# Performance work log

Measured on AMD Instinct MI355X. Metric: run time of the kernel, lower is better.

Reference implementation:

```python
import jax, jax.numpy as jnp
import numpy as np

H = 256        # hidden_size
MAX_LEN = 200  # position table has MAX_LEN+1 rows
B = 4096       # number of sessions


def setup_inputs() -> dict:
    rng = np.random.RandomState(0)
    # ragged session lengths in [10, 100)
    seq_len = rng.randint(10, 100, size=B).astype(np.int64)
    T = int(seq_len.sum())
    # reverse positions: len-1, ..., 1, 0 per session (as the torch code uses)
    reverse_pos = np.concatenate([np.arange(l - 1, -1, -1) for l in seq_len]).astype(np.int64)

    key = jax.random.key(0)
    ks = jax.random.split(key, 8)
    def lin(k, fin, fout):
        # torch Linear init ~ U(-1/sqrt(fin), 1/sqrt(fin)); store as [fin, fout]
        lim = 1.0 / np.sqrt(fin)
        kw, kb = jax.random.split(k)
        W = jax.random.uniform(kw, (fin, fout), jnp.float32, -lim, lim)
        b = jax.random.uniform(kb, (fout,), jnp.float32, -lim, lim)
        return W, b

    hidden = jax.random.normal(ks[0], (T, H), jnp.float32)
    pos_table = jax.random.normal(ks[1], (MAX_LEN + 1, H), jnp.float32)
    W_pos, b_pos = lin(ks[2], 2 * H, H)   # W_pos_inter
    W1, b1 = lin(ks[3], H, H)             # W_1_inter
    W2, b2 = lin(ks[4], H, H)             # W_2_inter
    qw, qb = lin(ks[5], H, 1)             # q_inter

    return {
        "hidden": hidden,
        "pos_table": pos_table,
        "W_pos": W_pos, "b_pos": b_pos,
        "W1": W1, "b1": b1,
        "W2": W2, "b2": b2,
        "qw": qw, "qb": qb,
        "seq_len": jnp.asarray(seq_len),
        "reverse_pos": jnp.asarray(reverse_pos),
    }


def reference(hidden, pos_table, W_pos, b_pos, W1, b1, W2, b2, qw, qb, seq_len, reverse_pos):
    T = hidden.shape[0]
    nb = seq_len.shape[0]
    # segment id per token (sessions are contiguous)
    seg = jnp.repeat(jnp.arange(nb), seq_len, total_repeat_length=T)  # [T]
    # per-session mean, gathered back per token (v_mean_repeat_concat)
    sess_mean = jax.ops.segment_sum(hidden, seg, num_segments=nb)
    sess_mean = sess_mean / seq_len[:, None].astype(hidden.dtype)
    v_mean = sess_mean[seg]                                           # [T, H]
    # position-augmented hidden: tanh(W_pos_inter([hidden; pos_emb]))
    pos_emb = pos_table[reverse_pos]                                  # [T, H]
    pos_hidden = jnp.tanh(jnp.concatenate([hidden, pos_emb], -1) @ W_pos + b_pos)
    # alpha = q_inter(sigmoid(W_1_inter(v_mean) + W_2_inter(pos_hidden)))
    gate = jax.nn.sigmoid(v_mean @ W1 + b1 + pos_hidden @ W2 + b2)
    alpha = gate @ qw + qb                                            # [T, 1]
    # per-session weighted sum of hidden
    h_s = jax.ops.segment_sum(alpha * hidden, seg, num_segments=nb)   # [B, H]
    return h_s
```

## Files before the change

### kernel.cpp

```cpp
#include <hip/hip_runtime.h>
#include <hip/hip_bf16.h>
#include <stdint.h>

#define HD 256
#define BM 128
#define MAXS 16
#define APAD 8
#define ASTRIDE (HD + APAD)
#define USTRIDE (HD + 4)

typedef __bf16 bf16x8 __attribute__((ext_vector_type(8)));
typedef float f32x4 __attribute__((ext_vector_type(4)));
typedef unsigned short ushort8v __attribute__((ext_vector_type(8)));
typedef unsigned short us4 __attribute__((ext_vector_type(4)));

__device__ __forceinline__ unsigned short f2bf(float f) {
    unsigned int x = __float_as_uint(f);
    unsigned int r = (x + 0x7FFFu + ((x >> 16) & 1u)) >> 16;
    return (unsigned short)r;
}
__device__ __forceinline__ float bf2f(unsigned short u) {
    return __uint_as_float(((unsigned)u) << 16);
}

__global__ void prep_kernel(const int* __restrict__ seq_len, int* __restrict__ offsets, int B,
                            int* __restrict__ grp_off, int* __restrict__ grp_meta,
                            const float* __restrict__ Wp, const float* __restrict__ W1,
                            const float* __restrict__ W2,
                            unsigned short* __restrict__ WphT, unsigned short* __restrict__ WpbT,
                            unsigned short* __restrict__ W1T, unsigned short* __restrict__ W2T) {
    int tid = threadIdx.x;
    if (blockIdx.x == 0) {
        __shared__ int sums[256];
        int per = (B + 255) / 256;
        int b0 = tid * per;
        int local[32];
        int tot = 0;
        for (int i = 0; i < per && i < 32; ++i) {
            int b = b0 + i;
            int v = (b < B) ? seq_len[b] : 0;
            local[i] = tot;
            tot += v;
        }
        sums[tid] = tot;
        __syncthreads();
        for (int off = 1; off < 256; off <<= 1) {
            int v = (tid >= off) ? sums[tid - off] : 0;
            __syncthreads();
            sums[tid] += v;
            __syncthreads();
        }
        int start = sums[tid] - tot;
        for (int i = 0; i < per && i < 32; ++i) {
            int b = b0 + i;
            if (b < B) offsets[b] = start + local[i];
        }
        if (tid == 255) offsets[B] = sums[255];

        int starts[32];
        int ng = 0;
        {
            int cur = 0, cnt = 0;
            for (int i = 0; i < per && i < 32; ++i) {
                int b = b0 + i;
                if (b >= B) break;
                int nxt = (i + 1 < per && i + 1 < 32) ? local[i + 1] : tot;
                int len = nxt - local[i];
                if (i == 0 || cur + len > BM || cnt == MAXS) { starts[ng++] = b; cur = 0; cnt = 0; }
                cur += len; cnt++;
            }
        }
        __syncthreads();
        sums[tid] = ng;
        __syncthreads();
        for (int off = 1; off < 256; off <<= 1) {
            int v = (tid >= off) ? sums[tid - off] : 0;
            __syncthreads();
            sums[tid] += v;
            __syncthreads();
        }
        int gbase = sums[tid] - ng;
        for (int j = 0; j < ng; ++j) grp_off[gbase + j] = starts[j];
        if (tid == 255) { grp_meta[0] = sums[255]; grp_off[sums[255]] = B; }
    } else {
        __shared__ unsigned short tile[64][72];
        int bid = blockIdx.x - 1;
        const float* src;
        unsigned short* dst;
        int k0, n0, kk;
        if (bid < 32) {
            int tk = bid >> 2, tn = bid & 3;
            src = Wp; k0 = tk * 64; n0 = tn * 64;
            if (k0 < 256) { dst = WphT; kk = k0; }
            else          { dst = WpbT; kk = k0 - 256; }
        } else if (bid < 48) {
            int b2 = bid - 32;
            src = W1; k0 = (b2 >> 2) * 64; n0 = (b2 & 3) * 64;
            dst = W1T; kk = k0;
        } else {
            int b2 = bid - 48;
            src = W2; k0 = (b2 >> 2) * 64; n0 = (b2 & 3) * 64;
            dst = W2T; kk = k0;
        }
        {
            int col = tid & 63;
            int rbase = tid >> 6;
            #pragma unroll
            for (int i = 0; i < 16; ++i) {
                int lrow = rbase + 4 * i;
                tile[lrow][col] = f2bf(src[(size_t)(k0 + lrow) * HD + n0 + col]);
            }
        }
        __syncthreads();
        {
            int nl = tid >> 2;
            int kc0 = (tid & 3) * 16;
            #pragma unroll
            for (int j = 0; j < 4; ++j) {
                int kc = kc0 + 4 * j;
                us4 v;
                v[0] = tile[kc + 0][nl];
                v[1] = tile[kc + 1][nl];
                v[2] = tile[kc + 2][nl];
                v[3] = tile[kc + 3][nl];
                *reinterpret_cast<us4*>(dst + (size_t)(n0 + nl) * HD + kk + kc) = v;
            }
        }
    }
}

__global__ __launch_bounds__(256) void p2_kernel(
    const float* __restrict__ pos_table, int Mp,
    const unsigned short* __restrict__ WpbT, const float* __restrict__ bp,
    float* __restrict__ P2) {
    __shared__ __align__(16) unsigned short As[16][ASTRIDE];
    int tid = threadIdx.x;
    int m0 = blockIdx.x * 16;
    {
        int row = tid >> 4;
        int colg = (tid & 15) * 16;
        int m = m0 + row;
        float4 f[4] = {{0,0,0,0},{0,0,0,0},{0,0,0,0},{0,0,0,0}};
        if (m < Mp) {
            const float4* p = reinterpret_cast<const float4*>(pos_table + (size_t)m * HD + colg);
            f[0] = p[0]; f[1] = p[1]; f[2] = p[2]; f[3] = p[3];
        }
        ushort8v v0, v1;
        v0[0]=f2bf(f[0].x); v0[1]=f2bf(f[0].y); v0[2]=f2bf(f[0].z); v0[3]=f2bf(f[0].w);
        v0[4]=f2bf(f[1].x); v0[5]=f2bf(f[1].y); v0[6]=f2bf(f[1].z); v0[7]=f2bf(f[1].w);
        v1[0]=f2bf(f[2].x); v1[1]=f2bf(f[2].y); v1[2]=f2bf(f[2].z); v1[3]=f2bf(f[2].w);
        v1[4]=f2bf(f[3].x); v1[5]=f2bf(f[3].y); v1[6]=f2bf(f[3].z); v1[7]=f2bf(f[3].w);
        *reinterpret_cast<ushort8v*>(&As[row][colg])     = v0;
        *reinterpret_cast<ushort8v*>(&As[row][colg + 8]) = v1;
    }
    __syncthreads();

    int wave = tid >> 6, lane = tid & 63, quad = lane >> 4, cc = lane & 15;
    int nb = wave * 64;
    f32x4 acc4[4];
    for (int i = 0; i < 4; ++i) acc4[i] = (f32x4){0.f, 0.f, 0.f, 0.f};
    bf16x8 wfp[4];
    for (int nf = 0; nf < 4; ++nf)
        wfp[nf] = *reinterpret_cast<const bf16x8*>(WpbT + (size_t)(nb + nf * 16 + cc) * HD + quad * 8);
    for (int kc8 = 0; kc8 < 8; ++kc8) {
        int kc = kc8 * 32;
        bf16x8 wfc[4];
        for (int nf = 0; nf < 4; ++nf) wfc[nf] = wfp[nf];
        if (kc8 < 7)
            for (int nf = 0; nf < 4; ++nf)
                wfp[nf] = *reinterpret_cast<const bf16x8*>(WpbT + (size_t)(nb + nf * 16 + cc) * HD + kc + 32 + quad * 8);
        bf16x8 af = *reinterpret_cast<const bf16x8*>(&As[cc][kc + quad * 8]);
        for (int nf = 0; nf < 4; ++nf)
            acc4[nf] = __builtin_amdgcn_mfma_f32_16x16x32_bf16(af, wfc[nf], acc4[nf], 0, 0, 0);
    }
    for (int nf = 0; nf < 4; ++nf)
        for (int r = 0; r < 4; ++r) {
            int row = m0 + quad * 4 + r;
            int col = nb + nf * 16 + cc;
            if (row < Mp) P2[(size_t)row * HD + col] = acc4[nf][r] + bp[col];
        }
}

__global__ __launch_bounds__(512, 4) void main_kernel(
    const float* __restrict__ hidden,
    const unsigned short* __restrict__ WphT,
    const unsigned short* __restrict__ W1T,
    const unsigned short* __restrict__ W2T,
    const float* __restrict__ P2,
    const float* __restrict__ b1, const float* __restrict__ b2,
    const float* __restrict__ qw, const float* __restrict__ qb,
    const int* __restrict__ rp, const int* __restrict__ offsets,
    const int* __restrict__ grp_off, const int* __restrict__ grp_meta,
    float* __restrict__ out) {
    __shared__ __align__(16) unsigned short Ah[BM][ASTRIDE];
    __shared__ __align__(16) unsigned short Ms[MAXS][ASTRIDE];
    __shared__ float alpha_s[BM];
    __shared__ int rp_s[BM];
    __shared__ int seg_l[BM];
    __shared__ int sess_st[MAXS + 1];

    int NG = grp_meta[0];
    if ((int)blockIdx.x >= NG) return;
    int tid = threadIdx.x;
    int b0  = grp_off[blockIdx.x];
    int b1e = grp_off[blockIdx.x + 1];
    int nsess = b1e - b0;
    int t0g = offsets[b0];
    int nrows = offsets[b1e] - t0g;

    int wv = tid >> 6, lane = tid & 63, quad = lane >> 4, cc = lane & 15;
    int mb = wv * 32;

    if (tid <= nsess) sess_st[tid] = offsets[b0 + tid] - t0g;
    if (tid < BM) {
        alpha_s[tid] = qb[0];
        rp_s[tid] = (tid < nrows) ? rp[t0g + tid] : 0;
    }

    bf16x8 afp[2];
    #pragma unroll
    for (int mf = 0; mf < 2; ++mf)
        afp[mf] = *reinterpret_cast<const bf16x8*>(WphT + (size_t)(mb + mf * 16 + cc) * HD + quad * 8);

    {
        int row = tid >> 2;
        #pragma unroll
        for (int i = 0; i < 8; ++i) {
            int cg = (tid & 3) * 8 + 32 * i;
            float4 f0 = {0,0,0,0}, f1 = {0,0,0,0};
            if (row < nrows) {
                const float4* p = reinterpret_cast<const float4*>(hidden + (size_t)(t0g + row) * HD + cg);
                f0 = p[0]; f1 = p[1];
            }
            ushort8v pk;
            pk[0] = f2bf(f0.x); pk[1] = f2bf(f0.y); pk[2] = f2bf(f0.z); pk[3] = f2bf(f0.w);
            pk[4] = f2bf(f1.x); pk[5] = f2bf(f1.y); pk[6] = f2bf(f1.z); pk[7] = f2bf(f1.w);
            *reinterpret_cast<ushort8v*>(&Ah[row][cg]) = pk;
        }
    }
    __syncthreads();

    if (tid < BM) {
        int s = 0;
        #pragma unroll
        for (int stp = 8; stp >= 1; stp >>= 1)
            if (s + stp < nsess && sess_st[s + stp] <= tid) s += stp;
        seg_l[tid] = (tid < nrows) ? s : 0;
    }
    for (int s = wv; s < nsess; s += 8) {
        int st = sess_st[s], en = sess_st[s + 1];
        float a0 = 0.f, a1 = 0.f, a2 = 0.f, a3 = 0.f;
        for (int r = st; r < en; ++r) {
            us4 v = *reinterpret_cast<const us4*>(&Ah[r][lane * 4]);
            a0 += bf2f(v[0]); a1 += bf2f(v[1]); a2 += bf2f(v[2]); a3 += bf2f(v[3]);
        }
        float inv = 1.0f / (float)(en - st);
        us4 pk;
        pk[0] = f2bf(a0 * inv); pk[1] = f2bf(a1 * inv);
        pk[2] = f2bf(a2 * inv); pk[3] = f2bf(a3 * inv);
        *reinterpret_cast<us4*>(&Ms[s][lane * 4]) = pk;
    }
    __syncthreads();

    f32x4 acc[2][8];
    #pragma unroll
    for (int i = 0; i < 2; ++i)
        #pragma unroll
        for (int j = 0; j < 8; ++j) acc[i][j] = (f32x4){0.f, 0.f, 0.f, 0.f};

    for (int kc8 = 0; kc8 < 8; ++kc8) {
        int kc = kc8 * 32;
        bf16x8 afc[2] = {afp[0], afp[1]};
        if (kc8 < 7)
            #pragma unroll
            for (int mf = 0; mf < 2; ++mf)
                afp[mf] = *reinterpret_cast<const bf16x8*>(WphT + (size_t)(mb + mf * 16 + cc) * HD + kc + 32 + quad * 8);
        #pragma unroll
        for (int nf = 0; nf < 8; ++nf) {
            bf16x8 bfr = *reinterpret_cast<const bf16x8*>(&Ah[nf * 16 + cc][kc + quad * 8]);
            acc[0][nf] = __builtin_amdgcn_mfma_f32_16x16x32_bf16(afc[0], bfr, acc[0][nf], 0, 0, 0);
            acc[1][nf] = __builtin_amdgcn_mfma_f32_16x16x32_bf16(afc[1], bfr, acc[1][nf], 0, 0, 0);
        }
    }

    f32x4 uacc[2];
    uacc[0] = (f32x4){0.f, 0.f, 0.f, 0.f};
    uacc[1] = (f32x4){0.f, 0.f, 0.f, 0.f};
    for (int kc8 = 0; kc8 < 8; ++kc8) {
        int kc = kc8 * 32;
        bf16x8 msf = *reinterpret_cast<const bf16x8*>(&Ms[cc][kc + quad * 8]);
        #pragma unroll
        for (int nf = 0; nf < 2; ++nf) {
            bf16x8 wf = *reinterpret_cast<const bf16x8*>(W1T + (size_t)(mb + nf * 16 + cc) * HD + kc + quad * 8);
            uacc[nf] = __builtin_amdgcn_mfma_f32_16x16x32_bf16(msf, wf, uacc[nf], 0, 0, 0);
        }
    }

    bf16x8 wfp[2];
    #pragma unroll
    for (int mf = 0; mf < 2; ++mf)
        wfp[mf] = *reinterpret_cast<const bf16x8*>(W2T + (size_t)(mb + mf * 16 + cc) * HD + quad * 8);
    __syncthreads();

    #pragma unroll
    for (int nf = 0; nf < 8; ++nf) {
        int token = nf * 16 + cc;
        const float* p2row = P2 + (size_t)rp_s[token] * HD;
        #pragma unroll
        for (int mf = 0; mf < 2; ++mf) {
            int h0 = mb + mf * 16 + quad * 4;
            const f32x4 p2v = *reinterpret_cast<const f32x4*>(p2row + h0);
            us4 pk;
            {
                float v0 = acc[mf][nf][0] + p2v[0];
                float v1 = acc[mf][nf][1] + p2v[1];
                float v2 = acc[mf][nf][2] + p2v[2];
                float v3 = acc[mf][nf][3] + p2v[3];
                float e0 = __expf(2.f * v0), e1 = __expf(2.f * v1);
                float e2 = __expf(2.f * v2), e3 = __expf(2.f * v3);
                pk[0] = f2bf(1.f - 2.f / (e0 + 1.f));
                pk[1] = f2bf(1.f - 2.f / (e1 + 1.f));
                pk[2] = f2bf(1.f - 2.f / (e2 + 1.f));
                pk[3] = f2bf(1.f - 2.f / (e3 + 1.f));
            }
            *reinterpret_cast<us4*>(&Ah[token][h0]) = pk;
            acc[mf][nf] = (f32x4){0.f, 0.f, 0.f, 0.f};
        }
    }
    __syncthreads();

    for (int kc8 = 0; kc8 < 8; ++kc8) {
        int kc = kc8 * 32;
        bf16x8 wfc[2] = {wfp[0], wfp[1]};
        if (kc8 < 7)
            #pragma unroll
            for (int mf = 0; mf < 2; ++mf)
                wfp[mf] = *reinterpret_cast<const bf16x8*>(W2T + (size_t)(mb + mf * 16 + cc) * HD + kc + 32 + quad * 8);
        #pragma unroll
        for (int nf = 0; nf < 8; ++nf) {
            bf16x8 af = *reinterpret_cast<const bf16x8*>(&Ah[nf * 16 + cc][kc + quad * 8]);
            acc[0][nf] = __builtin_amdgcn_mfma_f32_16x16x32_bf16(wfc[0], af, acc[0][nf], 0, 0, 0);
            acc[1][nf] = __builtin_amdgcn_mfma_f32_16x16x32_bf16(wfc[1], af, acc[1][nf], 0, 0, 0);
        }
    }
    __syncthreads();

    float* usp = reinterpret_cast<float*>(&Ah[0][0]);
    {
        #pragma unroll
        for (int nf = 0; nf < 2; ++nf) {
            int n = mb + nf * 16 + cc;
            float b12 = b1[n] + b2[n];
            #pragma unroll
            for (int r = 0; r < 4; ++r)
                usp[(quad * 4 + r) * USTRIDE + n] = uacc[nf][r] + b12;
        }
    }
    __syncthreads();

    f32x4 qv[2];
    #pragma unroll
    for (int mf = 0; mf < 2; ++mf)
        qv[mf] = *reinterpret_cast<const f32x4*>(qw + mb + mf * 16 + quad * 4);
    #pragma unroll
    for (int nf = 0; nf < 8; ++nf) {
        int token = nf * 16 + cc;
        int stok = seg_l[token];
        float s = 0.f;
        #pragma unroll
        for (int mf = 0; mf < 2; ++mf) {
            const f32x4 uv = *reinterpret_cast<const f32x4*>(&usp[stok * USTRIDE + mb + mf * 16 + quad * 4]);
            #pragma unroll
            for (int r = 0; r < 4; ++r) {
                float g = acc[mf][nf][r] + uv[r];
                g = 1.0f / (1.0f + __expf(-g));
                s += g * qv[mf][r];
            }
        }
        s += __shfl_xor(s, 16);
        s += __shfl_xor(s, 32);
        if (quad == 0) atomicAdd(&alpha_s[token], s);
    }
    __syncthreads();

    {
        int col = tid & 255, p = tid >> 8;
        const float* hp = hidden + (size_t)t0g * HD + col;
        for (int si = p; si < nsess; si += 2) {
            int st = sess_st[si], en = sess_st[si + 1];
            float a0 = 0.f, a1 = 0.f;
            int r = st;
            for (; r + 1 < en; r += 2) {
                a0 += alpha_s[r]     * hp[(size_t)r * HD];
                a1 += alpha_s[r + 1] * hp[(size_t)(r + 1) * HD];
            }
            if (r < en) a0 += alpha_s[r] * hp[(size_t)r * HD];
            out[(size_t)(b0 + si) * HD + col] = a0 + a1;
        }
    }
}

extern "C" void kernel_launch(void* const* d_in, const int* in_sizes, int n_in,
                              void* d_out, int out_size, void* d_ws, size_t ws_size,
                              hipStream_t stream) {
    (void)n_in; (void)out_size; (void)ws_size;
    const float* hidden    = (const float*)d_in[0];
    const float* pos_table = (const float*)d_in[1];
    const float* W_pos     = (const float*)d_in[2];
    const float* b_pos     = (const float*)d_in[3];
    const float* W1        = (const float*)d_in[4];
    const float* b1        = (const float*)d_in[5];
    const float* W2        = (const float*)d_in[6];
    const float* b2        = (const float*)d_in[7];
    const float* qw        = (const float*)d_in[8];
    const float* qb        = (const float*)d_in[9];
    const int* seq_len     = (const int*)d_in[10];
    const int* reverse_pos = (const int*)d_in[11];

    int B  = in_sizes[10];
    int NP = in_sizes[1] / HD;

    char* ws = (char*)d_ws;
    auto carve = [&](size_t bytes) -> char* {
        char* p = ws;
        ws += (bytes + 255) & ~(size_t)255;
        return p;
    };
    int* offsets          = (int*)carve((size_t)(B + 1) * sizeof(int));
    int* grp_off          = (int*)carve((size_t)(B + 2) * sizeof(int));
    int* grp_meta         = (int*)carve(64);
    float* P2             = (float*)carve((size_t)NP * HD * sizeof(float));
    unsigned short* WphT  = (unsigned short*)carve((size_t)HD * HD * 2);
    unsigned short* WpbT  = (unsigned short*)carve((size_t)HD * HD * 2);
    unsigned short* W1T   = (unsigned short*)carve((size_t)HD * HD * 2);
    unsigned short* W2T   = (unsigned short*)carve((size_t)HD * HD * 2);

    prep_kernel<<<65, 256, 0, stream>>>(seq_len, offsets, B, grp_off, grp_meta,
                                        W_pos, W1, W2, WphT, WpbT, W1T, W2T);
    p2_kernel<<<(NP + 15) / 16, 256, 0, stream>>>(pos_table, NP, WpbT, b_pos, P2);
    main_kernel<<<B, 512, 0, stream>>>(hidden, WphT, W1T, W2T, P2, b1, b2, qw, qb,
                                       reverse_pos, offsets, grp_off, grp_meta,
                                       (float*)d_out);
}
```

Measured before the change: 569.0 us.

## Retile MFMA warps to token×hidden blocks and overlap first GEMM with session mean

Each of the 8 waves now owns a 32-token by 128-hidden tile instead of a 32-hidden by 128-token tile. B fragments come from LDS with only 2 loads per k-step, and weight fragments are read straight from global/L2. The first GEMM moves ahead of the session-mean loop so both run before a single barrier, dropping one sync. The mean and final weighted-sum loops are also unrolled with more independent accumulators to shorten the dependency chains. The cost is 8 global weight loads per k-step per wave with no prefetch, and unrolled loops that may raise register pressure.

Result: slower. 737.9 us (+29.7%).

```diff
diff --git a/kernel.cpp b/kernel.cpp
--- a/kernel.cpp
+++ b/kernel.cpp
@@ -209,18 +209,15 @@
     int nrows = offsets[b1e] - t0g;
 
     int wv = tid >> 6, lane = tid & 63, quad = lane >> 4, cc = lane & 15;
-    int mb = wv * 32;
+    int tg = wv & 3, hh = wv >> 2;
+    int tokb = tg * 32;
+    int hb   = hh * 128;
 
     if (tid <= nsess) sess_st[tid] = offsets[b0 + tid] - t0g;
     if (tid < BM) {
         alpha_s[tid] = qb[0];
         rp_s[tid] = (tid < nrows) ? rp[t0g + tid] : 0;
     }
-
-    bf16x8 afp[2];
-    #pragma unroll
-    for (int mf = 0; mf < 2; ++mf)
-        afp[mf] = *reinterpret_cast<const bf16x8*>(WphT + (size_t)(mb + mf * 16 + cc) * HD + quad * 8);
 
     {
         int row = tid >> 2;
@@ -247,75 +244,78 @@
             if (s + stp < nsess && sess_st[s + stp] <= tid) s += stp;
         seg_l[tid] = (tid < nrows) ? s : 0;
     }
+
+    f32x4 acc[8][2];
+    #pragma unroll
+    for (int i = 0; i < 8; ++i) {
+        acc[i][0] = (f32x4){0.f, 0.f, 0.f, 0.f};
+        acc[i][1] = (f32x4){0.f, 0.f, 0.f, 0.f};
+    }
+
+    #pragma unroll
+    for (int kc8 = 0; kc8 < 8; ++kc8) {
+        int kc = kc8 * 32;
+        bf16x8 bf0 = *reinterpret_cast<const bf16x8*>(&Ah[tokb + cc][kc + quad * 8]);
+        bf16x8 bf1 = *reinterpret_cast<const bf16x8*>(&Ah[tokb + 16 + cc][kc + quad * 8]);
+        #pragma unroll
+        for (int hf = 0; hf < 8; ++hf) {
+            bf16x8 wf = *reinterpret_cast<const bf16x8*>(WphT + (size_t)(hb + hf * 16 + cc) * HD + kc + quad * 8);
+            acc[hf][0] = __builtin_amdgcn_mfma_f32_16x16x32_bf16(wf, bf0, acc[hf][0], 0, 0, 0);
+            acc[hf][1] = __builtin_amdgcn_mfma_f32_16x16x32_bf16(wf, bf1, acc[hf][1], 0, 0, 0);
+        }
+    }
+
     for (int s = wv; s < nsess; s += 8) {
         int st = sess_st[s], en = sess_st[s + 1];
         float a0 = 0.f, a1 = 0.f, a2 = 0.f, a3 = 0.f;
-        for (int r = st; r < en; ++r) {
+        float c0 = 0.f, c1 = 0.f, c2 = 0.f, c3 = 0.f;
+        int r = st;
+        for (; r + 1 < en; r += 2) {
+            us4 v = *reinterpret_cast<const us4*>(&Ah[r][lane * 4]);
+            us4 w = *reinterpret_cast<const us4*>(&Ah[r + 1][lane * 4]);
+            a0 += bf2f(v[0]); a1 += bf2f(v[1]); a2 += bf2f(v[2]); a3 += bf2f(v[3]);
+            c0 += bf2f(w[0]); c1 += bf2f(w[1]); c2 += bf2f(w[2]); c3 += bf2f(w[3]);
+        }
+        if (r < en) {
             us4 v = *reinterpret_cast<const us4*>(&Ah[r][lane * 4]);
             a0 += bf2f(v[0]); a1 += bf2f(v[1]); a2 += bf2f(v[2]); a3 += bf2f(v[3]);
         }
         float inv = 1.0f / (float)(en - st);
         us4 pk;
-        pk[0] = f2bf(a0 * inv); pk[1] = f2bf(a1 * inv);
-        pk[2] = f2bf(a2 * inv); pk[3] = f2bf(a3 * inv);
+        pk[0] = f2bf((a0 + c0) * inv); pk[1] = f2bf((a1 + c1) * inv);
+        pk[2] = f2bf((a2 + c2) * inv); pk[3] = f2bf((a3 + c3) * inv);
         *reinterpret_cast<us4*>(&Ms[s][lane * 4]) = pk;
     }
     __syncthreads();
-
-    f32x4 acc[2][8];
-    #pragma unroll
-    for (int i = 0; i < 2; ++i)
-        #pragma unroll
-        for (int j = 0; j < 8; ++j) acc[i][j] = (f32x4){0.f, 0.f, 0.f, 0.f};
-
-    for (int kc8 = 0; kc8 < 8; ++kc8) {
-        int kc = kc8 * 32;
-        bf16x8 afc[2] = {afp[0], afp[1]};
-        if (kc8 < 7)
-            #pragma unroll
-            for (int mf = 0; mf < 2; ++mf)
-                afp[mf] = *reinterpret_cast<const bf16x8*>(WphT + (size_t)(mb + mf * 16 + cc) * HD + kc + 32 + quad * 8);
-        #pragma unroll
-        for (int nf = 0; nf < 8; ++nf) {
-            bf16x8 bfr = *reinterpret_cast<const bf16x8*>(&Ah[nf * 16 + cc][kc + quad * 8]);
-            acc[0][nf] = __builtin_amdgcn_mfma_f32_16x16x32_bf16(afc[0], bfr, acc[0][nf], 0, 0, 0);
-            acc[1][nf] = __builtin_amdgcn_mfma_f32_16x16x32_bf16(afc[1], bfr, acc[1][nf], 0, 0, 0);
-        }
-    }
 
     f32x4 uacc[2];
     uacc[0] = (f32x4){0.f, 0.f, 0.f, 0.f};
     uacc[1] = (f32x4){0.f, 0.f, 0.f, 0.f};
+    #pragma unroll
     for (int kc8 = 0; kc8 < 8; ++kc8) {
         int kc = kc8 * 32;
         bf16x8 msf = *reinterpret_cast<const bf16x8*>(&Ms[cc][kc + quad * 8]);
         #pragma unroll
         for (int nf = 0; nf < 2; ++nf) {
-            bf16x8 wf = *reinterpret_cast<const bf16x8*>(W1T + (size_t)(mb + nf * 16 + cc) * HD + kc + quad * 8);
+            bf16x8 wf = *reinterpret_cast<const bf16x8*>(W1T + (size_t)(wv * 32 + nf * 16 + cc) * HD + kc + quad * 8);
             uacc[nf] = __builtin_amdgcn_mfma_f32_16x16x32_bf16(msf, wf, uacc[nf], 0, 0, 0);
         }
     }
 
-    bf16x8 wfp[2];
-    #pragma unroll
-    for (int mf = 0; mf < 2; ++mf)
-        wfp[mf] = *reinterpret_cast<const bf16x8*>(W2T + (size_t)(mb + mf * 16 + cc) * HD + quad * 8);
-    __syncthreads();
-
-    #pragma unroll
-    for (int nf = 0; nf < 8; ++nf) {
-        int token = nf * 16 + cc;
+    #pragma unroll
+    for (int nf = 0; nf < 2; ++nf) {
+        int token = tokb + nf * 16 + cc;
         const float* p2row = P2 + (size_t)rp_s[token] * HD;
         #pragma unroll
-        for (int mf = 0; mf < 2; ++mf) {
-            int h0 = mb + mf * 16 + quad * 4;
+        for (int hf = 0; hf < 8; ++hf) {
+            int h0 = hb + hf * 16 + quad * 4;
             const f32x4 p2v = *reinterpret_cast<const f32x4*>(p2row + h0);
             us4 pk;
             {
-                float v0 = acc[mf][nf][0] + p2v[0];
-                float v1 = acc[mf][nf][1] + p2v[1];
-                float v2 = acc[mf][nf][2] + p2v[2];
-                float v3 = acc[mf][nf][3] + p2v[3];
+                float v0 = acc[hf][nf][0] + p2v[0];
+                float v1 = acc[hf][nf][1] + p2v[1];
+                float v2 = acc[hf][nf][2] + p2v[2];
+                float v3 = acc[hf][nf][3] + p2v[3];
                 float e0 = __expf(2.f * v0), e1 = __expf(2.f * v1);
                 float e2 = __expf(2.f * v2), e3 = __expf(2.f * v3);
                 pk[0] = f2bf(1.f - 2.f / (e0 + 1.f));
@@ -324,23 +324,21 @@
                 pk[3] = f2bf(1.f - 2.f / (e3 + 1.f));
             }
             *reinterpret_cast<us4*>(&Ah[token][h0]) = pk;
-            acc[mf][nf] = (f32x4){0.f, 0.f, 0.f, 0.f};
-        }
-    }
-    __syncthreads();
-
+            acc[hf][nf] = (f32x4){0.f, 0.f, 0.f, 0.f};
+        }
+    }
+    __syncthreads();
+
+    #pragma unroll
     for (int kc8 = 0; kc8 < 8; ++kc8) {
         int kc = kc8 * 32;
-        bf16x8 wfc[2] = {wfp[0], wfp[1]};
-        if (kc8 < 7)
-            #pragma unroll
-            for (int mf = 0; mf < 2; ++mf)
-                wfp[mf] = *reinterpret_cast<const bf16x8*>(W2T + (size_t)(mb + mf * 16 + cc) * HD + kc + 32 + quad * 8);
-        #pragma unroll
-        for (int nf = 0; nf < 8; ++nf) {
-            bf16x8 af = *reinterpret_cast<const bf16x8*>(&Ah[nf * 16 + cc][kc + quad * 8]);
-            acc[0][nf] = __builtin_amdgcn_mfma_f32_16x16x32_bf16(wfc[0], af, acc[0][nf], 0, 0, 0);
-            acc[1][nf] = __builtin_amdgcn_mfma_f32_16x16x32_bf16(wfc[1], af, acc[1][nf], 0, 0, 0);
+        bf16x8 bf0 = *reinterpret_cast<const bf16x8*>(&Ah[tokb + cc][kc + quad * 8]);
+        bf16x8 bf1 = *reinterpret_cast<const bf16x8*>(&Ah[tokb + 16 + cc][kc + quad * 8]);
+        #pragma unroll
+        for (int hf = 0; hf < 8; ++hf) {
+            bf16x8 wf = *reinterpret_cast<const bf16x8*>(W2T + (size_t)(hb + hf * 16 + cc) * HD + kc + quad * 8);
+            acc[hf][0] = __builtin_amdgcn_mfma_f32_16x16x32_bf16(wf, bf0, acc[hf][0], 0, 0, 0);
+            acc[hf][1] = __builtin_amdgcn_mfma_f32_16x16x32_bf16(wf, bf1, acc[hf][1], 0, 0, 0);
         }
     }
     __syncthreads();
@@ -349,7 +347,7 @@
     {
         #pragma unroll
         for (int nf = 0; nf < 2; ++nf) {
-            int n = mb + nf * 16 + cc;
+            int n = wv * 32 + nf * 16 + cc;
             float b12 = b1[n] + b2[n];
             #pragma unroll
             for (int r = 0; r < 4; ++r)
@@ -358,23 +356,21 @@
     }
     __syncthreads();
 
-    f32x4 qv[2];
-    #pragma unroll
-    for (int mf = 0; mf < 2; ++mf)
-        qv[mf] = *reinterpret_cast<const f32x4*>(qw + mb + mf * 16 + quad * 4);
-    #pragma unroll
-    for (int nf = 0; nf < 8; ++nf) {
-        int token = nf * 16 + cc;
+    #pragma unroll
+    for (int nf = 0; nf < 2; ++nf) {
+        int token = tokb + nf * 16 + cc;
         int stok = seg_l[token];
         float s = 0.f;
         #pragma unroll
-        for (int mf = 0; mf < 2; ++mf) {
-            const f32x4 uv = *reinterpret_cast<const f32x4*>(&usp[stok * USTRIDE + mb + mf * 16 + quad * 4]);
+        for (int hf = 0; hf < 8; ++hf) {
+            int n0 = hb + hf * 16 + quad * 4;
+            const f32x4 uv = *reinterpret_cast<const f32x4*>(&usp[stok * USTRIDE + n0]);
+            const f32x4 qv = *reinterpret_cast<const f32x4*>(qw + n0);
             #pragma unroll
             for (int r = 0; r < 4; ++r) {
-                float g = acc[mf][nf][r] + uv[r];
+                float g = acc[hf][nf][r] + uv[r];
                 g = 1.0f / (1.0f + __expf(-g));
-                s += g * qv[mf][r];
+                s += g * qv[r];
             }
         }
         s += __shfl_xor(s, 16);
@@ -388,14 +384,16 @@
         const float* hp = hidden + (size_t)t0g * HD + col;
         for (int si = p; si < nsess; si += 2) {
             int st = sess_st[si], en = sess_st[si + 1];
-            float a0 = 0.f, a1 = 0.f;
+            float a0 = 0.f, a1 = 0.f, a2 = 0.f, a3 = 0.f;
             int r = st;
-            for (; r + 1 < en; r += 2) {
+            for (; r + 3 < en; r += 4) {
                 a0 += alpha_s[r]     * hp[(size_t)r * HD];
                 a1 += alpha_s[r + 1] * hp[(size_t)(r + 1) * HD];
-            }
-            if (r < en) a0 += alpha_s[r] * hp[(size_t)r * HD];
-            out[(size_t)(b0 + si) * HD + col] = a0 + a1;
+                a2 += alpha_s[r + 2] * hp[(size_t)(r + 2) * HD];
+                a3 += alpha_s[r + 3] * hp[(size_t)(r + 3) * HD];
+            }
+            for (; r < en; ++r) a0 += alpha_s[r] * hp[(size_t)r * HD];
+            out[(size_t)(b0 + si) * HD + col] = (a0 + a1) + (a2 + a3);
         }
     }
 }
```
